# Performance work log

Hardware: AMD Instinct MI355X
Metric: run time of the kernel (lower is better)

The kernel has to match this reference:

```python
import jax, jax.numpy as jnp
import numpy as np

NUM_CLASSES = 8
NUM_MAPS = 4
FEAT_C = 2048  # ResNet-50 layer4 channels
HW = 14        # spatial size (448/32)


def setup_inputs() -> dict:
    key = jax.random.key(0)
    k1, k2, k3, k4, k5 = jax.random.split(key, 5)
    B = 64
    x = jax.random.normal(k1, (B, FEAT_C, HW, HW), dtype=jnp.float32)
    down_w = jax.random.normal(k2, (NUM_CLASSES * NUM_MAPS, FEAT_C), dtype=jnp.float32) * 0.02
    down_b = jax.random.normal(k3, (NUM_CLASSES * NUM_MAPS,), dtype=jnp.float32) * 0.02
    fc_w = jax.random.normal(k4, (NUM_CLASSES, 2 * FEAT_C), dtype=jnp.float32) * 0.02
    fc_b = jax.random.normal(k5, (NUM_CLASSES,), dtype=jnp.float32) * 0.02
    return {"x": x, "down_w": down_w, "down_b": down_b, "fc_w": fc_w, "fc_b": fc_b}


def reference(x, down_w, down_b, fc_w, fc_b):
    B = x.shape[0]
    x_ori = x  # [B, 2048, 14, 14] (ResNet features output)
    # downconv: 1x1 conv 2048 -> num_classes*num_maps
    xc = jnp.einsum('bchw,oc->bohw', x_ori, down_w) + down_b[None, :, None, None]  # [B,32,14,14]
    # GMP over full 14x14 window -> [B, 32]
    gmp = jnp.max(xc, axis=(2, 3))
    # spatial_pooling = ClassWisePool(num_maps): mean over groups of num_maps channels
    scores = gmp.reshape(B, NUM_CLASSES, NUM_MAPS).mean(axis=2)  # [B, 8]
    x_out = jax.nn.log_softmax(scores, axis=1)  # first output
    # class-wise pool on the full conv map: [B,32,14,14] -> [B,8,14,14]
    xcp = xc.reshape(B, NUM_CLASSES, NUM_MAPS, HW, HW).mean(axis=2)
    # modulate each class map by its (log-softmax) score
    xcp = xcp * x_out[:, :, None, None]
    # spatial_pooling2 = ClassWisePool(num_classes): mean over 8 class channels -> [B,1,14,14]
    sal = xcp.mean(axis=1, keepdims=True)
    prod = sal * x_ori  # [B,2048,14,14] via broadcast (fused, no copies)
    cat = jnp.concatenate([x_ori, prod], axis=1)  # [B,4096,14,14]
    # GAP 14x14 -> [B,4096]
    gap = cat.mean(axis=(2, 3))
    logits2 = gap @ fc_w.T + fc_b  # [B,8]
    x_conv_out = jax.nn.log_softmax(logits2, axis=1)
    return (x_out, x_conv_out)
```

## Files before the change

kernel.cpp:

```cpp
#include <hip/hip_runtime.h>

#define NCH 2048
#define HW 196
#define NB 64
#define NOUT 48
#define NCHUNK 8
#define CPC (NCH / NCHUNK)
#define KS_PER_BLK (CPC / 32)
#define KGTOT (NCH / 32)
#define NT 13
#define MT 3
#define TILE_F (32 * HW)
#define TILE_V4 (TILE_F / 4)
#define SLAB (NT * NOUT * 16)
#define SLAB4 (SLAB / 4)

typedef __attribute__((ext_vector_type(8))) short bf16x8;
typedef __attribute__((ext_vector_type(4))) float f32x4;
typedef __attribute__((ext_vector_type(4))) int i32x4;

__device__ __forceinline__ short f2bf(float f) {
    unsigned int u = __float_as_uint(f);
    u = u + 0x7fffu + ((u >> 16) & 1u);
    return (short)(u >> 16);
}

__global__ void build_afrag(const float* __restrict__ down_w,
                            const float* __restrict__ fc_w,
                            bf16x8* __restrict__ afrag) {
    int t = blockIdx.x * 256 + threadIdx.x;
    if (t >= KGTOT * MT * 64) return;
    int lane = t & 63;
    int frag = t >> 6;
    int mt = frag % MT;
    int kg = frag / MT;
    int o = mt * 16 + (lane & 15);
    int cbase = kg * 32 + (lane >> 4) * 8;
    bf16x8 v;
#pragma unroll
    for (int j = 0; j < 8; ++j) {
        int c = cbase + j;
        float w;
        if (o < 32)      w = down_w[o * NCH + c];
        else if (o < 40) w = fc_w[(o - 32) * (2 * NCH) + NCH + c];
        else             w = fc_w[(o - 40) * (2 * NCH) + c];
        v[j] = f2bf(w);
    }
    afrag[frag * 64 + lane] = v;
}

__global__ __launch_bounds__(256) void conv_mfma(const float* __restrict__ x,
                                                 const bf16x8* __restrict__ afrag,
                                                 float* __restrict__ part) {
    __shared__ float ldsx[2][TILE_F];
    const int chunk = blockIdx.x;
    const int b = blockIdx.y;
    const int tid = threadIdx.x;
    const int wave = tid >> 6;
    const int lane = tid & 63;
    const int nsub = lane & 15;
    const int kq = lane >> 4;

    f32x4 acc[4][MT];
#pragma unroll
    for (int i = 0; i < 4; ++i)
#pragma unroll
        for (int m = 0; m < MT; ++m)
            acc[i][m] = (f32x4){0.f, 0.f, 0.f, 0.f};

    int pidx[4];
#pragma unroll
    for (int i = 0; i < 4; ++i) {
        int p = (wave + 4 * i) * 16 + nsub;
        pidx[i] = (p < HW) ? p : (HW - 1);
    }

    const float* xtile0 = x + ((size_t)b * NCH + (size_t)chunk * CPC) * HW;

    auto stage = [&](int ks, int bb) {
        const float* g = xtile0 + (size_t)ks * TILE_F;
#pragma unroll
        for (int r = 0; r < 7; ++r) {
            int q = r * 256 + tid;
            if (q < TILE_V4) {
                __builtin_amdgcn_global_load_lds(
                    (const __attribute__((address_space(1))) unsigned int*)(g + (size_t)q * 4),
                    (__attribute__((address_space(3))) unsigned int*)(&ldsx[bb][(r * 256 + wave * 64) * 4]),
                    16, 0, 0);
            }
        }
    };

    stage(0, 0);

    for (int ks = 0; ks < KS_PER_BLK; ++ks) {
        __syncthreads();
        if (ks + 1 < KS_PER_BLK) stage(ks + 1, (ks + 1) & 1);

        const int kg = chunk * KS_PER_BLK + ks;
        bf16x8 a0 = afrag[(kg * MT + 0) * 64 + lane];
        bf16x8 a1 = afrag[(kg * MT + 1) * 64 + lane];
        bf16x8 a2 = afrag[(kg * MT + 2) * 64 + lane];

        const float* base = &ldsx[ks & 1][kq * 8 * HW];
#pragma unroll
        for (int i = 0; i < 4; ++i) {
            const float* bp = base + pidx[i];
            unsigned int u[8];
#pragma unroll
            for (int j = 0; j < 8; ++j)
                u[j] = __float_as_uint(bp[j * HW]) + 0x8000u;
            i32x4 bi;
            bi[0] = (int)__builtin_amdgcn_perm(u[1], u[0], 0x07060302u);
            bi[1] = (int)__builtin_amdgcn_perm(u[3], u[2], 0x07060302u);
            bi[2] = (int)__builtin_amdgcn_perm(u[5], u[4], 0x07060302u);
            bi[3] = (int)__builtin_amdgcn_perm(u[7], u[6], 0x07060302u);
            bf16x8 bv = __builtin_bit_cast(bf16x8, bi);
            acc[i][0] = __builtin_amdgcn_mfma_f32_16x16x32_bf16(a0, bv, acc[i][0], 0, 0, 0);
            acc[i][1] = __builtin_amdgcn_mfma_f32_16x16x32_bf16(a1, bv, acc[i][1], 0, 0, 0);
            acc[i][2] = __builtin_amdgcn_mfma_f32_16x16x32_bf16(a2, bv, acc[i][2], 0, 0, 0);
        }
    }

    float* pb = part + (size_t)(b * NCHUNK + chunk) * SLAB;
#pragma unroll
    for (int i = 0; i < 4; ++i) {
        int nt = wave + 4 * i;
        if (nt < NT) {
            float* d = pb + nt * (NOUT * 16) + kq * 64 + nsub;
#pragma unroll
            for (int m = 0; m < MT; ++m)
#pragma unroll
                for (int r = 0; r < 4; ++r)
                    d[m * 256 + r * 16] = acc[i][m][r];
        }
    }
}

__global__ __launch_bounds__(256) void finish(const float* __restrict__ part,
                                              const float* __restrict__ down_b,
                                              const float* __restrict__ fc_b,
                                              float* __restrict__ out) {
    const int b = blockIdx.x;
    const int tid = threadIdx.x;
    __shared__ float Ts[NOUT * HW];
    __shared__ float gmpS[32];
    __shared__ float scoreS[8];
    __shared__ float xoS[8];
    __shared__ float salS[HW];
    __shared__ float logitS[8];

    {
        const float4* base = (const float4*)(part + (size_t)b * NCHUNK * SLAB);
        for (int i4 = tid; i4 < SLAB4; i4 += 256) {
            float4 s = base[i4];
#pragma unroll
            for (int ch = 1; ch < NCHUNK; ++ch) {
                float4 v = base[(size_t)ch * SLAB4 + i4];
                s.x += v.x; s.y += v.y; s.z += v.z; s.w += v.w;
            }
            int nt = i4 / 192;
            int rem = i4 - nt * 192;
            int o = rem >> 2, ns4 = rem & 3;
            int p = nt * 16 + ns4 * 4;
            float vv[4] = {s.x, s.y, s.z, s.w};
#pragma unroll
            for (int q = 0; q < 4; ++q)
                if (p + q < HW) Ts[o * HW + p + q] = vv[q];
        }
    }
    __syncthreads();

    if (tid < 32) {
        float m = -1e30f;
        for (int p = 0; p < HW; ++p) m = fmaxf(m, Ts[tid * HW + p]);
        gmpS[tid] = m + down_b[tid];
    }
    __syncthreads();

    if (tid < 8)
        scoreS[tid] = 0.25f * (gmpS[4 * tid] + gmpS[4 * tid + 1] +
                               gmpS[4 * tid + 2] + gmpS[4 * tid + 3]);
    __syncthreads();

    if (tid < 8) {
        float m = -1e30f;
        for (int k = 0; k < 8; ++k) m = fmaxf(m, scoreS[k]);
        float se = 0.f;
        for (int k = 0; k < 8; ++k) se += expf(scoreS[k] - m);
        float xo = scoreS[tid] - m - logf(se);
        xoS[tid] = xo;
        out[b * 8 + tid] = xo;
    }
    __syncthreads();

    if (tid < HW) {
        float s = 0.f;
#pragma unroll
        for (int k = 0; k < 8; ++k) {
            float bs = down_b[4 * k] + down_b[4 * k + 1] +
                       down_b[4 * k + 2] + down_b[4 * k + 3];
            float rs = Ts[(4 * k) * HW + tid] + Ts[(4 * k + 1) * HW + tid] +
                       Ts[(4 * k + 2) * HW + tid] + Ts[(4 * k + 3) * HW + tid] + bs;
            s += xoS[k] * rs;
        }
        salS[tid] = s * (1.f / 32.f);
    }
    __syncthreads();

    if (tid < 8) {
        float t1 = 0.f, t2 = 0.f;
        for (int p = 0; p < HW; ++p) {
            t1 += Ts[(40 + tid) * HW + p];
            t2 += salS[p] * Ts[(32 + tid) * HW + p];
        }
        logitS[tid] = (t1 + t2) * (1.f / 196.f) + fc_b[tid];
    }
    __syncthreads();

    if (tid < 8) {
        float m = -1e30f;
        for (int k = 0; k < 8; ++k) m = fmaxf(m, logitS[k]);
        float se = 0.f;
        for (int k = 0; k < 8; ++k) se += expf(logitS[k] - m);
        out[NB * 8 + b * 8 + tid] = logitS[tid] - m - logf(se);
    }
}

extern "C" void kernel_launch(void* const* d_in, const int* in_sizes, int n_in,
                              void* d_out, int out_size, void* d_ws, size_t ws_size,
                              hipStream_t stream) {
    const float* x      = (const float*)d_in[0];
    const float* down_w = (const float*)d_in[1];
    const float* down_b = (const float*)d_in[2];
    const float* fc_w   = (const float*)d_in[3];
    const float* fc_b   = (const float*)d_in[4];
    float* out = (float*)d_out;

    bf16x8* afrag = (bf16x8*)d_ws;
    float* part = (float*)((char*)d_ws + (size_t)KGTOT * MT * 64 * 16);

    build_afrag<<<(KGTOT * MT * 64 + 255) / 256, 256, 0, stream>>>(down_w, fc_w, afrag);
    conv_mfma<<<dim3(NCHUNK, NB), 256, 0, stream>>>(x, afrag, part);
    finish<<<NB, 256, 0, stream>>>(part, down_b, fc_b, out);
}
```

Baseline: 183.9 us.

## Triple-buffer conv staging, preload A fragments, split reduction into separate kernel

The conv kernel moves to a three-deep LDS ring fed by global_load_lds, with explicit vmcnt waits and raw barriers, and preloads all of a block's A fragments into registers up front. The K permutation is changed so each lane reads channel pairs, and partial sums are written as vector stores in a new output-major layout. The cross-chunk partial reduction becomes its own wide kernel, and the finish kernel's max and dot-product loops are spread across all threads. The intent is to hide load latency, reduce LDS read conflicts and remove serial work from the finish kernel, at the cost of an extra launch, an extra round trip of the reduced partials through global memory, and higher register pressure.

Result: faster. 174.9 us (-4.9%).

```diff
diff --git a/kernel.cpp b/kernel.cpp
--- a/kernel.cpp
+++ b/kernel.cpp
@@ -12,8 +12,10 @@
 #define MT 3
 #define TILE_F (32 * HW)
 #define TILE_V4 (TILE_F / 4)
+#define TILE_PAD 7168
 #define SLAB (NT * NOUT * 16)
 #define SLAB4 (SLAB / 4)
+#define ROWSTRIDE (16 * NOUT)
 
 typedef __attribute__((ext_vector_type(8))) short bf16x8;
 typedef __attribute__((ext_vector_type(4))) float f32x4;
@@ -35,11 +37,11 @@
     int mt = frag % MT;
     int kg = frag / MT;
     int o = mt * 16 + (lane & 15);
-    int cbase = kg * 32 + (lane >> 4) * 8;
+    int kq = lane >> 4;
     bf16x8 v;
 #pragma unroll
     for (int j = 0; j < 8; ++j) {
-        int c = cbase + j;
+        int c = kg * 32 + kq * 2 + (j & 1) + ((j >> 1) << 3);
         float w;
         if (o < 32)      w = down_w[o * NCH + c];
         else if (o < 40) w = fc_w[(o - 32) * (2 * NCH) + NCH + c];
@@ -49,10 +51,11 @@
     afrag[frag * 64 + lane] = v;
 }
 
-__global__ __launch_bounds__(256) void conv_mfma(const float* __restrict__ x,
-                                                 const bf16x8* __restrict__ afrag,
-                                                 float* __restrict__ part) {
-    __shared__ float ldsx[2][TILE_F];
+__global__ __launch_bounds__(256, 1) void conv(const float* __restrict__ x,
+                                               const bf16x8* __restrict__ afrag,
+                                               float* __restrict__ part) {
+    __shared__ float ldsx[3][TILE_PAD];
+
     const int chunk = blockIdx.x;
     const int b = blockIdx.y;
     const int tid = threadIdx.x;
@@ -82,43 +85,49 @@
 #pragma unroll
         for (int r = 0; r < 7; ++r) {
             int q = r * 256 + tid;
-            if (q < TILE_V4) {
-                __builtin_amdgcn_global_load_lds(
-                    (const __attribute__((address_space(1))) unsigned int*)(g + (size_t)q * 4),
-                    (__attribute__((address_space(3))) unsigned int*)(&ldsx[bb][(r * 256 + wave * 64) * 4]),
-                    16, 0, 0);
-            }
+            int qc = (q < TILE_V4) ? q : (TILE_V4 - 1);
+            __builtin_amdgcn_global_load_lds(
+                (const __attribute__((address_space(1))) unsigned int*)(g + (size_t)qc * 4),
+                (__attribute__((address_space(3))) unsigned int*)(&ldsx[bb][(r * 256 + wave * 64) * 4]),
+                16, 0, 0);
         }
     };
 
+    bf16x8 areg[KS_PER_BLK][MT];
+#pragma unroll
+    for (int ks = 0; ks < KS_PER_BLK; ++ks)
+#pragma unroll
+        for (int m = 0; m < MT; ++m)
+            areg[ks][m] = afrag[((chunk * KS_PER_BLK + ks) * MT + m) * 64 + lane];
+    __builtin_amdgcn_sched_barrier(0);
+
     stage(0, 0);
-
+    stage(1, 1);
+
+#pragma unroll
     for (int ks = 0; ks < KS_PER_BLK; ++ks) {
-        __syncthreads();
-        if (ks + 1 < KS_PER_BLK) stage(ks + 1, (ks + 1) & 1);
-
-        const int kg = chunk * KS_PER_BLK + ks;
-        bf16x8 a0 = afrag[(kg * MT + 0) * 64 + lane];
-        bf16x8 a1 = afrag[(kg * MT + 1) * 64 + lane];
-        bf16x8 a2 = afrag[(kg * MT + 2) * 64 + lane];
-
-        const float* base = &ldsx[ks & 1][kq * 8 * HW];
+        if (ks < KS_PER_BLK - 1) asm volatile("s_waitcnt vmcnt(7)" ::: "memory");
+        else                     asm volatile("s_waitcnt vmcnt(0)" ::: "memory");
+        __builtin_amdgcn_s_barrier();
+        if (ks + 2 < KS_PER_BLK) stage(ks + 2, (ks + 2) % 3);
+
+        const float* base = &ldsx[ks % 3][kq * 2 * HW];
 #pragma unroll
         for (int i = 0; i < 4; ++i) {
             const float* bp = base + pidx[i];
             unsigned int u[8];
 #pragma unroll
             for (int j = 0; j < 8; ++j)
-                u[j] = __float_as_uint(bp[j * HW]) + 0x8000u;
+                u[j] = __float_as_uint(bp[((j & 1) + ((j >> 1) << 3)) * HW]) + 0x8000u;
             i32x4 bi;
             bi[0] = (int)__builtin_amdgcn_perm(u[1], u[0], 0x07060302u);
             bi[1] = (int)__builtin_amdgcn_perm(u[3], u[2], 0x07060302u);
             bi[2] = (int)__builtin_amdgcn_perm(u[5], u[4], 0x07060302u);
             bi[3] = (int)__builtin_amdgcn_perm(u[7], u[6], 0x07060302u);
             bf16x8 bv = __builtin_bit_cast(bf16x8, bi);
-            acc[i][0] = __builtin_amdgcn_mfma_f32_16x16x32_bf16(a0, bv, acc[i][0], 0, 0, 0);
-            acc[i][1] = __builtin_amdgcn_mfma_f32_16x16x32_bf16(a1, bv, acc[i][1], 0, 0, 0);
-            acc[i][2] = __builtin_amdgcn_mfma_f32_16x16x32_bf16(a2, bv, acc[i][2], 0, 0, 0);
+            acc[i][0] = __builtin_amdgcn_mfma_f32_16x16x32_bf16(areg[ks][0], bv, acc[i][0], 0, 0, 0);
+            acc[i][1] = __builtin_amdgcn_mfma_f32_16x16x32_bf16(areg[ks][1], bv, acc[i][1], 0, 0, 0);
+            acc[i][2] = __builtin_amdgcn_mfma_f32_16x16x32_bf16(areg[ks][2], bv, acc[i][2], 0, 0, 0);
         }
     }
 
@@ -127,23 +136,38 @@
     for (int i = 0; i < 4; ++i) {
         int nt = wave + 4 * i;
         if (nt < NT) {
-            float* d = pb + nt * (NOUT * 16) + kq * 64 + nsub;
+            float* d = pb + nt * ROWSTRIDE + nsub * NOUT + kq * 4;
 #pragma unroll
             for (int m = 0; m < MT; ++m)
-#pragma unroll
-                for (int r = 0; r < 4; ++r)
-                    d[m * 256 + r * 16] = acc[i][m][r];
-        }
-    }
-}
-
-__global__ __launch_bounds__(256) void finish(const float* __restrict__ part,
+                *(f32x4*)(d + m * 16) = acc[i][m];
+        }
+    }
+}
+
+__global__ __launch_bounds__(256) void reduce_part(const float4* __restrict__ part4,
+                                                   float4* __restrict__ tred4) {
+    int t = blockIdx.x * 256 + threadIdx.x;
+    if (t >= NB * SLAB4) return;
+    int b = t / SLAB4;
+    int r = t - b * SLAB4;
+    const float4* p = part4 + (size_t)b * NCHUNK * SLAB4 + r;
+    float4 s = p[0];
+#pragma unroll
+    for (int ch = 1; ch < NCHUNK; ++ch) {
+        float4 v = p[(size_t)ch * SLAB4];
+        s.x += v.x; s.y += v.y; s.z += v.z; s.w += v.w;
+    }
+    tred4[t] = s;
+}
+
+__global__ __launch_bounds__(256) void finish(const float4* __restrict__ tred4,
                                               const float* __restrict__ down_b,
                                               const float* __restrict__ fc_b,
                                               float* __restrict__ out) {
     const int b = blockIdx.x;
     const int tid = threadIdx.x;
     __shared__ float Ts[NOUT * HW];
+    __shared__ float red[256];
     __shared__ float gmpS[32];
     __shared__ float scoreS[8];
     __shared__ float xoS[8];
@@ -151,29 +175,36 @@
     __shared__ float logitS[8];
 
     {
-        const float4* base = (const float4*)(part + (size_t)b * NCHUNK * SLAB);
+        const float4* basep = tred4 + (size_t)b * SLAB4;
         for (int i4 = tid; i4 < SLAB4; i4 += 256) {
-            float4 s = base[i4];
-#pragma unroll
-            for (int ch = 1; ch < NCHUNK; ++ch) {
-                float4 v = base[(size_t)ch * SLAB4 + i4];
-                s.x += v.x; s.y += v.y; s.z += v.z; s.w += v.w;
+            float4 s = basep[i4];
+            int idx = i4 * 4;
+            int ntv = idx / ROWSTRIDE;
+            int rem = idx - ntv * ROWSTRIDE;
+            int ns = rem / NOUT;
+            int o0 = rem - ns * NOUT;
+            int p = ntv * 16 + ns;
+            if (p < HW) {
+                Ts[o0 * HW + p] = s.x;
+                Ts[(o0 + 1) * HW + p] = s.y;
+                Ts[(o0 + 2) * HW + p] = s.z;
+                Ts[(o0 + 3) * HW + p] = s.w;
             }
-            int nt = i4 / 192;
-            int rem = i4 - nt * 192;
-            int o = rem >> 2, ns4 = rem & 3;
-            int p = nt * 16 + ns4 * 4;
-            float vv[4] = {s.x, s.y, s.z, s.w};
-#pragma unroll
-            for (int q = 0; q < 4; ++q)
-                if (p + q < HW) Ts[o * HW + p + q] = vv[q];
-        }
-    }
-    __syncthreads();
-
+        }
+    }
+    __syncthreads();
+
+    {
+        int o = tid >> 3, s8 = tid & 7;
+        float m = -1e30f;
+        for (int p = s8; p < HW; p += 8) m = fmaxf(m, Ts[o * HW + p]);
+        red[tid] = m;
+    }
+    __syncthreads();
     if (tid < 32) {
-        float m = -1e30f;
-        for (int p = 0; p < HW; ++p) m = fmaxf(m, Ts[tid * HW + p]);
+        float m = red[tid * 8];
+#pragma unroll
+        for (int j = 1; j < 8; ++j) m = fmaxf(m, red[tid * 8 + j]);
         gmpS[tid] = m + down_b[tid];
     }
     __syncthreads();
@@ -208,13 +239,19 @@
     }
     __syncthreads();
 
+    {
+        int c = tid >> 5, s32 = tid & 31;
+        float t = 0.f;
+        for (int p = s32; p < HW; p += 32)
+            t += Ts[(40 + c) * HW + p] + salS[p] * Ts[(32 + c) * HW + p];
+        red[tid] = t;
+    }
+    __syncthreads();
     if (tid < 8) {
-        float t1 = 0.f, t2 = 0.f;
-        for (int p = 0; p < HW; ++p) {
-            t1 += Ts[(40 + tid) * HW + p];
-            t2 += salS[p] * Ts[(32 + tid) * HW + p];
-        }
-        logitS[tid] = (t1 + t2) * (1.f / 196.f) + fc_b[tid];
+        float t = 0.f;
+#pragma unroll
+        for (int j = 0; j < 32; ++j) t += red[tid * 32 + j];
+        logitS[tid] = t * (1.f / 196.f) + fc_b[tid];
     }
     __syncthreads();
 
@@ -239,8 +276,10 @@
 
     bf16x8* afrag = (bf16x8*)d_ws;
     float* part = (float*)((char*)d_ws + (size_t)KGTOT * MT * 64 * 16);
+    float* tred = (float*)((char*)part + (size_t)NB * NCHUNK * SLAB * 4);
 
     build_afrag<<<(KGTOT * MT * 64 + 255) / 256, 256, 0, stream>>>(down_w, fc_w, afrag);
-    conv_mfma<<<dim3(NCHUNK, NB), 256, 0, stream>>>(x, afrag, part);
-    finish<<<NB, 256, 0, stream>>>(part, down_b, fc_b, out);
-}
+    conv<<<dim3(NCHUNK, NB), 256, 0, stream>>>(x, afrag, part);
+    reduce_part<<<(NB * SLAB4 + 255) / 256, 256, 0, stream>>>((const float4*)part, (float4*)tred);
+    finish<<<NB, 256, 0, stream>>>((const float4*)tred, down_b, fc_b, out);
+}
```
